# Performance work log

Hardware: AMD Instinct MI355X
Metric: run time of the kernel (lower is better)

The kernel has to match this reference:

```python
import jax, jax.numpy as jnp
import numpy as np

# --- static anchor geometry (exactly mirrors RPN._make_anchor_box) ---

def _valid_idx():
    scales = [64.0, 128.0, 256.0]
    ratios = [0.5, 1.0, 2.0]
    # (h, w) per anchor, normalized by 448
    anc = np.array([[s / np.sqrt(r), s * np.sqrt(r)] for s in scales for r in ratios]) / 448.0
    c = (np.arange(28) + 0.5) / 28.0
    cy = np.repeat(c, 28).reshape(28, 28)  # y varies along rows
    cx = np.tile(c, (28, 1))               # x varies along cols
    boxes = np.zeros((28, 28, 36))
    for a in range(9):
        boxes[..., 4 * a + 0] = cy
        boxes[..., 4 * a + 1] = cx
        boxes[..., 4 * a + 2] = anc[a, 0]
        boxes[..., 4 * a + 3] = anc[a, 1]
    b = boxes.reshape(-1, 4)  # [7056, 4] in yxhw
    y1 = b[:, 0] - b[:, 2] / 2
    x1 = b[:, 1] - b[:, 3] / 2
    y2 = b[:, 0] + b[:, 2] / 2
    x2 = b[:, 1] + b[:, 3] / 2
    return np.where((y1 > 0) & (x1 > 0) & (y2 < 28) & (x2 < 28))[0]

_VALID = _valid_idx()  # 4850 static indices

ROI_CLS_THRESHOLD = 0.9


def setup_inputs() -> dict:
    key = jax.random.key(0)
    ks = jax.random.split(key, 4)
    C = 2048
    return {
        'x': jax.random.normal(ks[0], (1, C, 28, 28), jnp.float32),
        'conv_w': jax.random.normal(ks[1], (C, C, 3, 3), jnp.float32) * 0.02,
        'conv_b': jnp.zeros((C,), jnp.float32),
        'reg_w': jax.random.normal(ks[2], (36, C), jnp.float32) * 0.02,
        'reg_b': jnp.zeros((36,), jnp.float32),
        'cls_w': jax.random.normal(ks[3], (9, C), jnp.float32) * 0.02,
        'cls_b': jnp.zeros((9,), jnp.float32),
    }


def reference(x, conv_w, conv_b, reg_w, reg_b, cls_w, cls_b):
    # Conv block: 3x3 conv + BatchNorm(identity at init: gamma=1, beta=0, running stats 0/1) + ReLU
    h = jax.lax.conv_general_dilated(
        x, conv_w, window_strides=(1, 1), padding=((1, 1), (1, 1)),
        dimension_numbers=('NCHW', 'OIHW', 'NCHW'))
    h = jax.nn.relu(h + conv_b[None, :, None, None])
    # 1x1 conv heads + sigmoid
    reg = jax.nn.sigmoid(jnp.einsum('bchw,oc->bohw', h, reg_w) + reg_b[None, :, None, None])  # [1,36,28,28]
    cls = jax.nn.sigmoid(jnp.einsum('bchw,oc->bohw', h, cls_w) + cls_b[None, :, None, None])  # [1,9,28,28]
    # exact replication of view/permute/squeeze + static valid-anchor gather
    reg = reg.reshape(1, 4, -1).transpose(0, 2, 1)[0][_VALID]  # [4850, 4]
    cls = cls.reshape(-1)[_VALID]                              # [4850]
    # inference path (gt=None): reg[cls > 0.9]; fixed-shape masked equivalent
    keep = cls > ROI_CLS_THRESHOLD
    return reg * keep[:, None]
```

## Files before the change

kernel.cpp:

```cpp
#include <hip/hip_runtime.h>
#include <cstdint>

typedef __attribute__((ext_vector_type(8))) short s8v;
typedef __attribute__((ext_vector_type(4))) float f4v;

__device__ __forceinline__ unsigned short bf16_rne(float f) {
    unsigned u = __float_as_uint(f);
    u += 0x7FFFu + ((u >> 16) & 1u);
    return (unsigned short)(u >> 16);
}
__device__ __forceinline__ float bf16f(unsigned short h) {
    return __uint_as_float(((unsigned)h) << 16);
}
__device__ __forceinline__ void cvt2(float a, float b, unsigned& hiw, unsigned& low) {
    unsigned ua = __float_as_uint(a), ub = __float_as_uint(b);
    unsigned ha = ua + 0x7FFFu + ((ua >> 16) & 1u);
    unsigned hb = ub + 0x7FFFu + ((ub >> 16) & 1u);
    hiw = (ha >> 16) | (hb & 0xFFFF0000u);
    float ra = a - __uint_as_float(ha & 0xFFFF0000u);
    float rb = b - __uint_as_float(hb & 0xFFFF0000u);
    unsigned la = __float_as_uint(ra), lb = __float_as_uint(rb);
    la += 0x7FFFu + ((la >> 16) & 1u);
    lb += 0x7FFFu + ((lb >> 16) & 1u);
    low = (la >> 16) | (lb & 0xFFFF0000u);
}
__device__ __forceinline__ void cvt2t(float a, float b, unsigned& hiw, unsigned& low) {
    unsigned ua = __float_as_uint(a), ub = __float_as_uint(b);
    hiw = (ua >> 16) | (ub & 0xFFFF0000u);
    float ra = a - __uint_as_float(ua & 0xFFFF0000u);
    float rb = b - __uint_as_float(ub & 0xFFFF0000u);
    unsigned la = __float_as_uint(ra), lb = __float_as_uint(rb);
    low = (la >> 16) | (lb & 0xFFFF0000u);
}
__device__ __forceinline__ void cvt8(float4 a, float4 b, s8v& hi, s8v& lo) {
    unsigned h0, h1, h2, h3, l0, l1, l2, l3;
    cvt2t(a.x, a.y, h0, l0);
    cvt2t(a.z, a.w, h1, l1);
    cvt2t(b.x, b.y, h2, l2);
    cvt2t(b.z, b.w, h3, l3);
    uint4 uh{h0, h1, h2, h3}, ul{l0, l1, l2, l3};
    hi = *(s8v*)&uh;
    lo = *(s8v*)&ul;
}

__global__ __launch_bounds__(256) void transpose_x(const float* __restrict__ x,
                                                   float* __restrict__ xt) {
    __shared__ float t[64][65];
    int c0 = blockIdx.x * 64, p0 = blockIdx.y * 64;
    int l = threadIdx.x & 63, g = threadIdx.x >> 6;
#pragma unroll
    for (int j = 0; j < 16; ++j) {
        int cc = j * 4 + g;
        int p = p0 + l;
        t[cc][l] = (p < 784) ? x[(size_t)(c0 + cc) * 784 + p] : 0.f;
    }
    __syncthreads();
#pragma unroll
    for (int j = 0; j < 16; ++j) {
        int pp = j * 4 + g;
        int p = p0 + pp;
        if (p < 784) xt[(size_t)p * 2048 + c0 + l] = t[l][pp];
    }
}

__global__ __launch_bounds__(256) void build_B(const float* __restrict__ xt,
                                               unsigned* __restrict__ Bhi,
                                               unsigned* __restrict__ Blo) {
    int p = blockIdx.x;
    int h = p / 28, w = p % 28;
#pragma unroll
    for (int it = 0; it < 4; ++it) {
        int cp = it * 256 + threadIdx.x;
        float va[18];
#pragma unroll
        for (int r = 0; r < 9; ++r) {
            int h2 = h + r / 3 - 1, w2 = w + r % 3 - 1;
            bool ok = (h2 >= 0) & (h2 < 28) & (w2 >= 0) & (w2 < 28);
            float2 v = ok ? ((const float2*)(xt + (size_t)(h2 * 28 + w2) * 2048))[cp]
                          : float2{0.f, 0.f};
            va[r] = v.x;
            va[9 + r] = v.y;
        }
        size_t base = (size_t)p * 9216 + (size_t)cp * 9;
#pragma unroll
        for (int d = 0; d < 9; ++d) {
            unsigned hw, lw;
            cvt2(va[2 * d], va[2 * d + 1], hw, lw);
            Bhi[base + d] = hw;
            Blo[base + d] = lw;
        }
    }
}

#define KCH 1152
#define NSTEP 36
#define LDS_BYTES 28672

__global__ __launch_bounds__(256, 4) void conv_gemm(const float* __restrict__ cw,
                                                    const char* __restrict__ wsb,
                                                    uint32_t offBhi, uint32_t offBlo,
                                                    float* __restrict__ part) {
    __shared__ char smem[LDS_BYTES];
    int tid = threadIdx.x;
    int lane = tid & 63, wave = tid >> 6;
    int bm0 = blockIdx.x * 128, bn0 = blockIdx.y * 112, z = blockIdx.z;

    uint32_t doff[4], dldsB[4];
#pragma unroll
    for (int j = 0; j < 4; ++j) {
        int i = j * 4 + wave;
        if (i >= 14) i -= 2;
        bool hiP = i < 7;
        int jj = hiP ? i : i - 7;
        int prow = jj * 16 + (lane >> 2);
        int pos = lane & 3;
        int gblk = pos ^ ((prow >> 1) & 3);
        uint32_t elem = (uint32_t)(bn0 + prow) * 18432 + (uint32_t)z * KCH + gblk * 8;
        doff[j] = (hiP ? offBhi : offBlo) + elem * 2;
        dldsB[j] = (hiP ? 0u : 7168u) + (uint32_t)jj * 1024;
    }

    int m = lane & 15, qd = lane >> 4;
    int sw = (m >> 1) & 3;
    uint32_t bpos = (uint32_t)m * 64 + (uint32_t)((qd ^ sw) * 16);

    const float4* ap0 = (const float4*)(cw + (size_t)(bm0 + wave * 32 + m) * 18432
                                        + (size_t)z * KCH + (size_t)qd * 8);
    const float4* ap1 = (const float4*)(cw + (size_t)(bm0 + wave * 32 + 16 + m) * 18432
                                        + (size_t)z * KCH + (size_t)qd * 8);

    f4v acc[2][7];
#pragma unroll
    for (int a = 0; a < 2; ++a)
#pragma unroll
        for (int b = 0; b < 7; ++b) acc[a][b] = f4v{0.f, 0.f, 0.f, 0.f};

#pragma unroll
    for (int j = 0; j < 4; ++j) {
        __builtin_amdgcn_global_load_lds(
            (const __attribute__((address_space(1))) void*)(wsb + doff[j]),
            (__attribute__((address_space(3))) void*)(smem + dldsB[j]), 16, 0, 0);
        doff[j] += 64;
    }
    s8v ah[2], al[2], ahn[2], aln[2];
    {
        float4 a0 = ap0[0], a1 = ap0[1], a2 = ap1[0], a3 = ap1[1];
        ap0 += 8;
        ap1 += 8;
        cvt8(a0, a1, ah[0], al[0]);
        cvt8(a2, a3, ah[1], al[1]);
    }
    __syncthreads();

#pragma unroll 2
    for (int step = 0; step < NSTEP; ++step) {
        char* smB = smem + (step & 1) * 14336;
        float4 a0, a1, a2, a3;
        if (step < NSTEP - 1) {
            char* smBn = smem + ((step & 1) ^ 1) * 14336;
#pragma unroll
            for (int j = 0; j < 4; ++j) {
                __builtin_amdgcn_global_load_lds(
                    (const __attribute__((address_space(1))) void*)(wsb + doff[j]),
                    (__attribute__((address_space(3))) void*)(smBn + dldsB[j]), 16, 0, 0);
                doff[j] += 64;
            }
            a0 = ap0[0];
            a1 = ap0[1];
            a2 = ap1[0];
            a3 = ap1[1];
            ap0 += 8;
            ap1 += 8;
        }

        __builtin_amdgcn_s_setprio(1);
#pragma unroll
        for (int nt = 0; nt < 7; ++nt) {
            s8v bh = *(const s8v*)(smB + bpos + nt * 1024);
            s8v bl = *(const s8v*)(smB + 7168 + bpos + nt * 1024);
#pragma unroll
            for (int mt = 0; mt < 2; ++mt) {
                acc[mt][nt] = __builtin_amdgcn_mfma_f32_16x16x32_bf16(ah[mt], bh, acc[mt][nt], 0, 0, 0);
                acc[mt][nt] = __builtin_amdgcn_mfma_f32_16x16x32_bf16(ah[mt], bl, acc[mt][nt], 0, 0, 0);
                acc[mt][nt] = __builtin_amdgcn_mfma_f32_16x16x32_bf16(al[mt], bh, acc[mt][nt], 0, 0, 0);
            }
        }
        __builtin_amdgcn_s_setprio(0);

        if (step < NSTEP - 1) {
            cvt8(a0, a1, ahn[0], aln[0]);
            cvt8(a2, a3, ahn[1], aln[1]);
        }
        __syncthreads();
        ah[0] = ahn[0];
        ah[1] = ahn[1];
        al[0] = aln[0];
        al[1] = aln[1];
    }

    float* pz = part + (size_t)z * 1605632;
#pragma unroll
    for (int mt = 0; mt < 2; ++mt) {
        int o = bm0 + wave * 32 + mt * 16 + qd * 4;
#pragma unroll
        for (int nt = 0; nt < 7; ++nt) {
            int p = bn0 + nt * 16 + m;
            *(float4*)(pz + (size_t)p * 2048 + o) =
                float4{acc[mt][nt].x, acc[mt][nt].y, acc[mt][nt].z, acc[mt][nt].w};
        }
    }
}

__constant__ int HMIN_d[9] = {3, 2, 1, 6, 4, 3, 11, 8, 6};
__constant__ int WMIN_d[9] = {1, 2, 3, 3, 4, 6, 6, 8, 11};

__global__ __launch_bounds__(256) void heads(const float* __restrict__ part,
                                             const float* __restrict__ conv_b,
                                             const float* __restrict__ reg_w,
                                             const float* __restrict__ reg_b,
                                             const float* __restrict__ cls_w,
                                             const float* __restrict__ cls_b,
                                             float* __restrict__ out) {
    int tid = threadIdx.x;
    int lane = tid & 63, wave = tid >> 6;
    int p = blockIdx.x;
    int ci = tid * 2;

    float4 h0 = ((const float4*)conv_b)[ci];
    float4 h1 = ((const float4*)conv_b)[ci + 1];
#pragma unroll
    for (int z = 0; z < 16; ++z) {
        const float4* pz = (const float4*)(part + (size_t)z * 1605632 + (size_t)p * 2048);
        float4 a = pz[ci], b = pz[ci + 1];
        h0.x += a.x; h0.y += a.y; h0.z += a.z; h0.w += a.w;
        h1.x += b.x; h1.y += b.y; h1.z += b.z; h1.w += b.w;
    }
    h0.x = fmaxf(h0.x, 0.f); h0.y = fmaxf(h0.y, 0.f);
    h0.z = fmaxf(h0.z, 0.f); h0.w = fmaxf(h0.w, 0.f);
    h1.x = fmaxf(h1.x, 0.f); h1.y = fmaxf(h1.y, 0.f);
    h1.z = fmaxf(h1.z, 0.f); h1.w = fmaxf(h1.w, 0.f);

    float s[45];
#pragma unroll
    for (int o = 0; o < 36; ++o) {
        float4 wa = ((const float4*)(reg_w + (size_t)o * 2048))[ci];
        float4 wb = ((const float4*)(reg_w + (size_t)o * 2048))[ci + 1];
        s[o] = h0.x * wa.x + h0.y * wa.y + h0.z * wa.z + h0.w * wa.w +
               h1.x * wb.x + h1.y * wb.y + h1.z * wb.z + h1.w * wb.w;
    }
#pragma unroll
    for (int a = 0; a < 9; ++a) {
        float4 wa = ((const float4*)(cls_w + (size_t)a * 2048))[ci];
        float4 wb = ((const float4*)(cls_w + (size_t)a * 2048))[ci + 1];
        s[36 + a] = h0.x * wa.x + h0.y * wa.y + h0.z * wa.z + h0.w * wa.w +
                    h1.x * wb.x + h1.y * wb.y + h1.z * wb.z + h1.w * wb.w;
    }

    __shared__ float wsum[4][45];
    __shared__ float fin[45];
#pragma unroll
    for (int o = 0; o < 45; ++o) {
        float v = s[o];
#pragma unroll
        for (int d = 1; d < 64; d <<= 1) v += __shfl_xor(v, d, 64);
        if (lane == 0) wsum[wave][o] = v;
    }
    __syncthreads();
    if (tid < 45) fin[tid] = wsum[0][tid] + wsum[1][tid] + wsum[2][tid] + wsum[3][tid];
    __syncthreads();

    if (tid < 9) {
        int ap = tid;
        int n = ap * 784 + p;
        int pix = n / 9, a2 = n % 9;
        int hh = pix / 28, ww = pix % 28;
        if (hh >= HMIN_d[a2] && ww >= WMIN_d[a2]) {
            int row = 0;
#pragma unroll
            for (int a3 = 0; a3 < 9; ++a3) {
                int hm = HMIN_d[a3], wm = WMIN_d[a3];
                int full = hh - hm; if (full < 0) full = 0;
                row += full * (28 - wm);
                if (hh >= hm) { int prt = ww - wm; if (prt < 0) prt = 0; row += prt; }
                if (a3 < a2 && hh >= hm && ww >= wm) row += 1;
            }
            float cl = fin[36 + ap] + cls_b[ap];
            float keep = (1.f / (1.f + expf(-cl)) > 0.9f) ? 1.f : 0.f;
#pragma unroll
            for (int q = 0; q < 4; ++q) {
                float rl = fin[q * 9 + ap] + reg_b[q * 9 + ap];
                out[row * 4 + q] = keep / (1.f + expf(-rl));
            }
        }
    }
}

extern "C" void kernel_launch(void* const* d_in, const int* in_sizes, int n_in,
                              void* d_out, int out_size, void* d_ws, size_t ws_size,
                              hipStream_t stream) {
    const float* x = (const float*)d_in[0];
    const float* conv_w = (const float*)d_in[1];
    const float* conv_b = (const float*)d_in[2];
    const float* reg_w = (const float*)d_in[3];
    const float* reg_b = (const float*)d_in[4];
    const float* cls_w = (const float*)d_in[5];
    const float* cls_b = (const float*)d_in[6];
    float* out = (float*)d_out;
    char* ws = (char*)d_ws;

    const size_t o_part = 0;
    const size_t o_xt = 0;
    const size_t o_Bhi = 102760448;
    const size_t o_Blo = 131661824;

    transpose_x<<<dim3(32, 13), 256, 0, stream>>>(x, (float*)(ws + o_xt));
    build_B<<<784, 256, 0, stream>>>((const float*)(ws + o_xt), (unsigned*)(ws + o_Bhi),
                                     (unsigned*)(ws + o_Blo));
    conv_gemm<<<dim3(16, 7, 16), 256, 0, stream>>>(conv_w, ws, (uint32_t)o_Bhi,
                                                   (uint32_t)o_Blo, (float*)(ws + o_part));
    heads<<<784, 256, 0, stream>>>((const float*)(ws + o_part), conv_b, reg_w, reg_b,
                                   cls_w, cls_b, out);
}
```

Measured before the change: 505.3 us.

## Triple-buffer LDS B tiles with two-step prefetch and explicit waitcnt scheduling

Converts the conv GEMM main loop from double-buffered LDS with one-step prefetch to a three-buffer ring, with both the B tile (global_load_lds) and the A fp32 operands prefetched two steps ahead. Manual vmcnt waits, raw s_barrier and sched_barrier calls replace __syncthreads so that outstanding loads can stay in flight across iterations. The goal is to hide global memory latency behind the MFMA cluster. The cost is more LDS (43 KB) and more registers, with launch bounds lowered from 4 to 3 blocks per CU, which reduces occupancy.

New measurement: 508.5 us. About the same (+0.6%).

```diff
diff --git a/kernel.cpp b/kernel.cpp
--- a/kernel.cpp
+++ b/kernel.cpp
@@ -94,9 +94,52 @@
 
 #define KCH 1152
 #define NSTEP 36
-#define LDS_BYTES 28672
-
-__global__ __launch_bounds__(256, 4) void conv_gemm(const float* __restrict__ cw,
+#define BUFB 14336
+#define LDS_BYTES 43008
+
+#define CONV_MFMA_CLUSTER()                                                              \
+    {                                                                                    \
+        const char* smB = (const char*)smem + rdo;                                       \
+        __builtin_amdgcn_s_setprio(1);                                                   \
+        _Pragma("unroll") for (int nt = 0; nt < 7; ++nt) {                               \
+            s8v bh = *(const s8v*)(smB + bpos + nt * 1024);                              \
+            s8v bl = *(const s8v*)(smB + 7168 + bpos + nt * 1024);                       \
+            _Pragma("unroll") for (int mt = 0; mt < 2; ++mt) {                           \
+                acc[mt][nt] =                                                            \
+                    __builtin_amdgcn_mfma_f32_16x16x32_bf16(ah[mt], bh, acc[mt][nt], 0, 0, 0); \
+                acc[mt][nt] =                                                            \
+                    __builtin_amdgcn_mfma_f32_16x16x32_bf16(ah[mt], bl, acc[mt][nt], 0, 0, 0); \
+                acc[mt][nt] =                                                            \
+                    __builtin_amdgcn_mfma_f32_16x16x32_bf16(al[mt], bh, acc[mt][nt], 0, 0, 0); \
+            }                                                                            \
+        }                                                                                \
+        __builtin_amdgcn_s_setprio(0);                                                   \
+    }
+
+#define CONV_STEP_FULL(ISS, CVT)                                                         \
+    {                                                                                    \
+        Araw[ISS][0] = ap0[0]; Araw[ISS][1] = ap0[1];                                    \
+        Araw[ISS][2] = ap1[0]; Araw[ISS][3] = ap1[1];                                    \
+        ap0 += 8; ap1 += 8;                                                              \
+        __builtin_amdgcn_sched_barrier(0);                                               \
+        _Pragma("unroll") for (int j = 0; j < 4; ++j) {                                  \
+            __builtin_amdgcn_global_load_lds(                                            \
+                (const __attribute__((address_space(1))) void*)(wsb + doff[j]),          \
+                (__attribute__((address_space(3))) void*)(smem + wro + dldsB[j]), 16, 0, 0); \
+            doff[j] += 64;                                                               \
+        }                                                                                \
+        __builtin_amdgcn_sched_barrier(0);                                               \
+        CONV_MFMA_CLUSTER();                                                             \
+        cvt8(Araw[CVT][0], Araw[CVT][1], ah[0], al[0]);                                  \
+        cvt8(Araw[CVT][2], Araw[CVT][3], ah[1], al[1]);                                  \
+        asm volatile("s_waitcnt vmcnt(8)" ::: "memory");                                 \
+        __builtin_amdgcn_s_barrier();                                                    \
+        __builtin_amdgcn_sched_barrier(0);                                               \
+        wro = rdo;                                                                       \
+        rdo = (rdo == 2u * BUFB) ? 0u : rdo + BUFB;                                      \
+    }
+
+__global__ __launch_bounds__(256, 3) void conv_gemm(const float* __restrict__ cw,
                                                     const char* __restrict__ wsb,
                                                     uint32_t offBhi, uint32_t offBlo,
                                                     float* __restrict__ part) {
@@ -135,6 +178,14 @@
 #pragma unroll
         for (int b = 0; b < 7; ++b) acc[a][b] = f4v{0.f, 0.f, 0.f, 0.f};
 
+    float4 Araw[2][4];
+    s8v ah[2], al[2];
+
+    Araw[0][0] = ap0[0]; Araw[0][1] = ap0[1]; Araw[0][2] = ap1[0]; Araw[0][3] = ap1[1];
+    ap0 += 8; ap1 += 8;
+    Araw[1][0] = ap0[0]; Araw[1][1] = ap0[1]; Araw[1][2] = ap1[0]; Araw[1][3] = ap1[1];
+    ap0 += 8; ap1 += 8;
+    __builtin_amdgcn_sched_barrier(0);
 #pragma unroll
     for (int j = 0; j < 4; ++j) {
         __builtin_amdgcn_global_load_lds(
@@ -142,60 +193,38 @@
             (__attribute__((address_space(3))) void*)(smem + dldsB[j]), 16, 0, 0);
         doff[j] += 64;
     }
-    s8v ah[2], al[2], ahn[2], aln[2];
+#pragma unroll
+    for (int j = 0; j < 4; ++j) {
+        __builtin_amdgcn_global_load_lds(
+            (const __attribute__((address_space(1))) void*)(wsb + doff[j]),
+            (__attribute__((address_space(3))) void*)(smem + BUFB + dldsB[j]), 16, 0, 0);
+        doff[j] += 64;
+    }
+    __builtin_amdgcn_sched_barrier(0);
+    cvt8(Araw[0][0], Araw[0][1], ah[0], al[0]);
+    cvt8(Araw[0][2], Araw[0][3], ah[1], al[1]);
+    asm volatile("s_waitcnt vmcnt(4)" ::: "memory");
+    __builtin_amdgcn_s_barrier();
+    __builtin_amdgcn_sched_barrier(0);
+
+    uint32_t rdo = 0, wro = 2u * BUFB;
+
+    for (int tt = 0; tt < NSTEP - 2; tt += 2) {
+        CONV_STEP_FULL(0, 1);
+        CONV_STEP_FULL(1, 0);
+    }
+
     {
-        float4 a0 = ap0[0], a1 = ap0[1], a2 = ap1[0], a3 = ap1[1];
-        ap0 += 8;
-        ap1 += 8;
-        cvt8(a0, a1, ah[0], al[0]);
-        cvt8(a2, a3, ah[1], al[1]);
-    }
-    __syncthreads();
-
-#pragma unroll 2
-    for (int step = 0; step < NSTEP; ++step) {
-        char* smB = smem + (step & 1) * 14336;
-        float4 a0, a1, a2, a3;
-        if (step < NSTEP - 1) {
-            char* smBn = smem + ((step & 1) ^ 1) * 14336;
-#pragma unroll
-            for (int j = 0; j < 4; ++j) {
-                __builtin_amdgcn_global_load_lds(
-                    (const __attribute__((address_space(1))) void*)(wsb + doff[j]),
-                    (__attribute__((address_space(3))) void*)(smBn + dldsB[j]), 16, 0, 0);
-                doff[j] += 64;
-            }
-            a0 = ap0[0];
-            a1 = ap0[1];
-            a2 = ap1[0];
-            a3 = ap1[1];
-            ap0 += 8;
-            ap1 += 8;
-        }
-
-        __builtin_amdgcn_s_setprio(1);
-#pragma unroll
-        for (int nt = 0; nt < 7; ++nt) {
-            s8v bh = *(const s8v*)(smB + bpos + nt * 1024);
-            s8v bl = *(const s8v*)(smB + 7168 + bpos + nt * 1024);
-#pragma unroll
-            for (int mt = 0; mt < 2; ++mt) {
-                acc[mt][nt] = __builtin_amdgcn_mfma_f32_16x16x32_bf16(ah[mt], bh, acc[mt][nt], 0, 0, 0);
-                acc[mt][nt] = __builtin_amdgcn_mfma_f32_16x16x32_bf16(ah[mt], bl, acc[mt][nt], 0, 0, 0);
-                acc[mt][nt] = __builtin_amdgcn_mfma_f32_16x16x32_bf16(al[mt], bh, acc[mt][nt], 0, 0, 0);
-            }
-        }
-        __builtin_amdgcn_s_setprio(0);
-
-        if (step < NSTEP - 1) {
-            cvt8(a0, a1, ahn[0], aln[0]);
-            cvt8(a2, a3, ahn[1], aln[1]);
-        }
-        __syncthreads();
-        ah[0] = ahn[0];
-        ah[1] = ahn[1];
-        al[0] = aln[0];
-        al[1] = aln[1];
+        CONV_MFMA_CLUSTER();
+        cvt8(Araw[1][0], Araw[1][1], ah[0], al[0]);
+        cvt8(Araw[1][2], Araw[1][3], ah[1], al[1]);
+        asm volatile("s_waitcnt vmcnt(0)" ::: "memory");
+        __builtin_amdgcn_s_barrier();
+        __builtin_amdgcn_sched_barrier(0);
+        rdo = (rdo == 2u * BUFB) ? 0u : rdo + BUFB;
+    }
+    {
+        CONV_MFMA_CLUSTER();
     }
 
     float* pz = part + (size_t)z * 1605632;
```
